# Performance work log

Measured on AMD Instinct MI355X. Metric: run time of the kernel, lower is better.

## Reference

```python
import jax, jax.numpy as jnp
import numpy as np


def _grouped_attn(q, k, v, mask, scale):
    # q: [T,H,D], k/v: [S,KH,D], mask: [T,S] or [KH,T,S] (True = visible)
    T, H, D = q.shape
    S, KH, _ = k.shape
    G = H // KH
    qg = q.reshape(T, KH, G, D)
    logits = jnp.einsum('tkgd,skd->kgts', qg, k) * scale
    if mask.ndim == 2:
        mask = jnp.broadcast_to(mask[None], (KH, T, S))
    logits = jnp.where(mask[:, None], logits, -1e30)
    p = jax.nn.softmax(logits, axis=-1)
    valid = mask.any(-1)  # [KH,T]: queries with at least one visible key
    p = jnp.where(valid[:, None, :, None], p, 0.0)
    o = jnp.einsum('kgts,skd->tkgd', p, v).reshape(T, H, D)
    return o, p


def setup_inputs() -> dict:
    key = jax.random.key(0)
    ks = jax.random.split(key, 4)
    T, H, KH, D = 2048, 16, 2, 128
    q = jax.random.normal(ks[0], (T, H, D), jnp.float32)
    k = jax.random.normal(ks[1], (T, KH, D), jnp.float32)
    v = jax.random.normal(ks[2], (T, KH, D), jnp.float32)
    w = jax.random.uniform(ks[3], (T, H, 3), jnp.float32)
    return dict(q=q, k=k, v=v, w=w, kernel_size=32, stride=16, block_size=64,
                top_n=16, num_init_blocks=1, num_local_blocks=2, window_size=512)


def reference(q, k, v, w, kernel_size, stride, block_size, top_n,
              num_init_blocks, num_local_blocks, window_size):
    T, H, D = q.shape
    KH = k.shape[1]
    scale = 1.0 / np.sqrt(D).astype(np.float32)
    t = jnp.arange(T)
    causal = t[None, :] <= t[:, None]  # [T,S]

    # ---- 1) compression: mean-pool overlapping windows of kernel_size / stride ----
    n_cmp = (T - kernel_size) // stride + 1
    starts = np.arange(n_cmp) * stride
    win_idx = starts[:, None] + np.arange(kernel_size)[None, :]  # [Ncmp,ks]
    cmp_k = k[win_idx].mean(axis=1)  # [Ncmp,KH,D]
    cmp_v = v[win_idx].mean(axis=1)
    j_end = jnp.asarray(starts) + kernel_size - 1
    cmp_mask = j_end[None, :] <= t[:, None]  # block fully in the past
    o_cmp, p_cmp = _grouped_attn(q, cmp_k, cmp_v, cmp_mask, scale)  # p_cmp [KH,G,T,Ncmp]

    # ---- 2) block selection from compressed attention probabilities ----
    n_blk = (T + block_size - 1) // block_size
    js, je = starts, starts + kernel_size
    bs_, be_ = np.arange(n_blk) * block_size, (np.arange(n_blk) + 1) * block_size
    M = jnp.asarray(((js[:, None] < be_[None, :]) & (bs_[None, :] < je[:, None])),
                    dtype=q.dtype)  # [Ncmp,Nblk] overlap indicator
    blk_score = jnp.einsum('kgtj,jb->ktb', p_cmp, M)  # sum over group heads

    b = jnp.arange(n_blk)
    t_blk = t // block_size
    forced = (b[None, :] < num_init_blocks) | \
             ((b[None, :] <= t_blk[:, None]) & (b[None, :] >= t_blk[:, None] - num_local_blocks + 1))
    blk_valid = (b[None, :] * block_size) <= t[:, None]
    score = jnp.where(forced[None], 1e30, blk_score)
    score = jnp.where(blk_valid[None], score, -1e30)
    _, idx = jax.lax.top_k(score, top_n)  # [KH,T,top_n]
    sel_blk = jax.nn.one_hot(idx, n_blk, dtype=q.dtype).sum(-2) > 0  # [KH,T,Nblk]

    # ---- 3) selected-block attention ----
    tok_sel = sel_blk[:, :, t // block_size]  # [KH,T,T]
    slc_mask = tok_sel & causal[None]
    o_slc, _ = _grouped_attn(q, k, v, slc_mask, scale)

    # ---- 4) sliding-window attention ----
    win_mask = causal & ((t[:, None] - t[None, :]) < window_size)
    o_win, _ = _grouped_attn(q, k, v, win_mask, scale)

    # ---- 5) gated combination ----
    o = w[..., 0:1] * o_cmp + w[..., 1:2] * o_slc + w[..., 2:3] * o_win
    return o
```

## Files before the change

kernel.cpp:

```cpp
#include <hip/hip_runtime.h>
#include <hip/hip_bf16.h>
#include <math.h>

#define T_ 2048
#define H_ 16
#define KH_ 2
#define G_ 8
#define D_ 128
#define NCMP 127
#define JP 128
#define NBLK 32
#define TOPN 16
#define WIN_ 512
#define SCALE 0.08838834764831845f

typedef __attribute__((ext_vector_type(8))) short short8;
typedef __attribute__((ext_vector_type(16))) float f32x16;

__device__ __forceinline__ unsigned short f2bf(float x) {
    union { float f; unsigned u; } c; c.f = x;
    unsigned u = c.u + 0x7fffu + ((c.u >> 16) & 1u);
    return (unsigned short)(u >> 16);
}
__device__ __forceinline__ float bf2f(unsigned short b) {
    union { unsigned u; float f; } c; c.u = (unsigned)b << 16; return c.f;
}

#define GLD16(gsrc, lds) \
    __builtin_amdgcn_global_load_lds( \
        (const __attribute__((address_space(1))) unsigned int*)(gsrc), \
        (__attribute__((address_space(3))) unsigned int*)(lds), 16, 0, 0)

__global__ __launch_bounds__(256) void prep_kv(
        const float* __restrict__ k, const float* __restrict__ v,
        unsigned short* __restrict__ kimg, unsigned short* __restrict__ vtimg) {
    const int b  = blockIdx.x;
    const int kh = blockIdx.y;
    const int s0 = b << 6;
    const int tid = threadIdx.x;
    const size_t tb = ((size_t)kh * 32 + b) * 8192;
#pragma unroll
    for (int it = 0; it < 4; ++it) {
        int idx = it * 256 + tid;
        int r = idx >> 4, c = idx & 15;
        const float* src = k + (size_t)(s0 + r) * (KH_ * D_) + kh * D_ + c * 8;
        float4 x = *reinterpret_cast<const float4*>(src);
        float4 y = *reinterpret_cast<const float4*>(src + 4);
        union { unsigned short u[8]; uint4 q; } o;
        o.u[0] = f2bf(x.x); o.u[1] = f2bf(x.y); o.u[2] = f2bf(x.z); o.u[3] = f2bf(x.w);
        o.u[4] = f2bf(y.x); o.u[5] = f2bf(y.y); o.u[6] = f2bf(y.z); o.u[7] = f2bf(y.w);
        *reinterpret_cast<uint4*>(&kimg[tb + r * 128 + ((c ^ (r & 7)) << 3)]) = o.q;
    }
#pragma unroll
    for (int it = 0; it < 4; ++it) {
        int idx = it * 256 + tid;
        int d = idx & 127, kc8 = idx >> 7;
        union { unsigned short u[8]; uint4 q; } o;
#pragma unroll
        for (int e = 0; e < 8; ++e)
            o.u[e] = f2bf(v[(size_t)(s0 + kc8 * 8 + e) * (KH_ * D_) + kh * D_ + d]);
        *reinterpret_cast<uint4*>(&vtimg[tb + d * 64 + ((kc8 ^ (d & 7)) << 3)]) = o.q;
    }
}

__global__ __launch_bounds__(128) void build_cmp(
        const float* __restrict__ k, const float* __restrict__ v,
        unsigned short* __restrict__ khiI, unsigned short* __restrict__ kloI,
        unsigned short* __restrict__ vflat) {
    int j  = blockIdx.x;
    int kh = blockIdx.y;
    int d  = threadIdx.x;
    unsigned short hb = 0, lb = 0, vb = 0;
    if (j < NCMP) {
        int s0 = j * 16;
        float sk = 0.f, sv = 0.f;
        for (int i = 0; i < 32; ++i) {
            sk += k[(size_t)(s0 + i) * KH_ * D_ + kh * D_ + d];
            sv += v[(size_t)(s0 + i) * KH_ * D_ + kh * D_ + d];
        }
        float mk = sk * (1.f / 32.f), mv = sv * (1.f / 32.f);
        hb = f2bf(mk);
        lb = f2bf(mk - bf2f(hb));
        vb = f2bf(mv);
    }
    int c = d >> 3;
    size_t ib = (size_t)kh * 16384 + j * 128 + ((c ^ (j & 7)) << 3) + (d & 7);
    khiI[ib] = hb;
    kloI[ib] = lb;
    vflat[(size_t)kh * 16384 + j * 128 + d] = vb;
}

__global__ __launch_bounds__(256) void prep_cmp_img(
        const unsigned short* __restrict__ vflat, unsigned short* __restrict__ cvtI) {
    const int kh = blockIdx.x;
    const int tid = threadIdx.x;
#pragma unroll
    for (int it = 0; it < 8; ++it) {
        int idx = it * 256 + tid;
        int d = idx & 127, jc8 = idx >> 7;
        union { unsigned short u[8]; uint4 q; } o;
#pragma unroll
        for (int e = 0; e < 8; ++e)
            o.u[e] = vflat[(size_t)kh * 16384 + (jc8 * 8 + e) * 128 + d];
        *reinterpret_cast<uint4*>(
            &cvtI[(size_t)kh * 16384 + d * 128 + ((jc8 ^ (d & 7)) << 3)]) = o.q;
    }
}

__global__ __launch_bounds__(256, 1) void cmp_attn_mfma(
        const float* __restrict__ q, const float* __restrict__ w,
        const unsigned short* __restrict__ khiI, const unsigned short* __restrict__ kloI,
        const unsigned short* __restrict__ cvtI,
        float* __restrict__ out, unsigned int* __restrict__ sel) {
    const int qt  = blockIdx.x;
    const int kh  = blockIdx.y;
    const int t0  = qt * 16;
    const int tid = threadIdx.x;
    const int wv  = tid >> 6;
    const int lane = tid & 63;
    const int l31 = lane & 31;
    const int hi  = lane >> 5;
    const int hi4 = hi * 4;

    __shared__ unsigned short KHI[JP * D_];
    __shared__ unsigned short KLO[JP * D_];
    __shared__ unsigned short CVT[JP * D_];
    __shared__ float wsc_s[16 * 132];
    __shared__ float bsc_s[16 * 32];
    __shared__ unsigned int sel_s[16];
    __shared__ float wfac[4][32];

    if (tid < 16) sel_s[tid] = 0u;
    for (int i = tid; i < 16 * 132; i += 256) wsc_s[i] = 0.f;

    const size_t cb = (size_t)kh * 16384;
#pragma unroll
    for (int it = 0; it < 8; ++it) {
        int off = (wv * 8 + it) * 512;
        GLD16(khiI + cb + off + lane * 8, &KHI[off]);
        GLD16(kloI + cb + off + lane * 8, &KLO[off]);
        GLD16(cvtI + cb + off + lane * 8, &CVT[off]);
    }

    const int qloc = l31 & 15;
    const int t    = t0 + qloc;
    const int h    = kh * G_ + 2 * wv + (l31 >> 4);
    short8 qhi[8], qlo[8];
    {
        const float* qrow = q + (size_t)t * (H_ * D_) + h * D_;
#pragma unroll
        for (int dc = 0; dc < 8; ++dc) {
            int d0 = dc * 16 + hi * 8;
            float4 x = *reinterpret_cast<const float4*>(qrow + d0);
            float4 y = *reinterpret_cast<const float4*>(qrow + d0 + 4);
            float e_[8] = {x.x, x.y, x.z, x.w, y.x, y.y, y.z, y.w};
            short8 fh, fl;
#pragma unroll
            for (int e = 0; e < 8; ++e) {
                unsigned short hb = f2bf(e_[e]);
                fh[e] = (short)hb;
                fl[e] = (short)f2bf(e_[e] - bf2f(hb));
            }
            qhi[dc] = fh; qlo[dc] = fl;
        }
    }
    __syncthreads();

    f32x16 s_[4];
#pragma unroll
    for (int tl = 0; tl < 4; ++tl)
#pragma unroll
        for (int r = 0; r < 16; ++r) s_[tl][r] = 0.f;
    __builtin_amdgcn_s_setprio(1);
#pragma unroll
    for (int dc = 0; dc < 8; ++dc) {
        int c8 = dc * 2 + hi;
        int swz = (c8 ^ (l31 & 7)) << 3;
#pragma unroll
        for (int tl = 0; tl < 4; ++tl) {
            int off = (tl * 32 + l31) * 128 + swz;
            short8 ahi = *reinterpret_cast<const short8*>(&KHI[off]);
            short8 alo = *reinterpret_cast<const short8*>(&KLO[off]);
            s_[tl] = __builtin_amdgcn_mfma_f32_32x32x16_bf16(ahi, qhi[dc], s_[tl], 0, 0, 0);
            s_[tl] = __builtin_amdgcn_mfma_f32_32x32x16_bf16(alo, qhi[dc], s_[tl], 0, 0, 0);
            s_[tl] = __builtin_amdgcn_mfma_f32_32x32x16_bf16(ahi, qlo[dc], s_[tl], 0, 0, 0);
        }
    }
    __builtin_amdgcn_s_setprio(0);

    const int nv = (t >= 31) ? (((t - 31) >> 4) + 1) : 0;
    float m = -1e30f;
#pragma unroll
    for (int tl = 0; tl < 4; ++tl)
#pragma unroll
        for (int r = 0; r < 16; ++r) {
            int j = tl * 32 + (r & 3) + 8 * (r >> 2) + hi4;
            float lg = (j < nv) ? s_[tl][r] * SCALE : -1e30f;
            s_[tl][r] = lg;
            m = fmaxf(m, lg);
        }
    m = fmaxf(m, __shfl_xor(m, 32));
    float lsum = 0.f;
#pragma unroll
    for (int tl = 0; tl < 4; ++tl)
#pragma unroll
        for (int r = 0; r < 16; ++r) {
            float e = __expf(s_[tl][r] - m);
            s_[tl][r] = e;
            lsum += e;
        }
    lsum += __shfl_xor(lsum, 32);
    const float linv = (nv > 0) ? 1.f / lsum : 0.f;

#pragma unroll
    for (int tl = 0; tl < 4; ++tl)
#pragma unroll
        for (int r = 0; r < 16; ++r) {
            int j = tl * 32 + (r & 3) + 8 * (r >> 2) + hi4;
            atomicAdd(&wsc_s[qloc * 132 + j], s_[tl][r] * linv);
        }

    f32x16 acc[4];
#pragma unroll
    for (int dt = 0; dt < 4; ++dt)
#pragma unroll
        for (int r = 0; r < 16; ++r) acc[dt][r] = 0.f;
#pragma unroll
    for (int kc = 0; kc < 8; ++kc) {
        const int su = kc >> 1, rb = (kc & 1) * 8;
        unsigned pa0, pa1, pb0, pb1;
        asm("v_cvt_pk_bf16_f32 %0, %1, %2" : "=v"(pa0) : "v"(s_[su][rb+0]), "v"(s_[su][rb+1]));
        asm("v_cvt_pk_bf16_f32 %0, %1, %2" : "=v"(pa1) : "v"(s_[su][rb+2]), "v"(s_[su][rb+3]));
        asm("v_cvt_pk_bf16_f32 %0, %1, %2" : "=v"(pb0) : "v"(s_[su][rb+4]), "v"(s_[su][rb+5]));
        asm("v_cvt_pk_bf16_f32 %0, %1, %2" : "=v"(pb1) : "v"(s_[su][rb+6]), "v"(s_[su][rb+7]));
        unsigned sa0 = __shfl_xor(pa0, 32);
        unsigned sa1 = __shfl_xor(pa1, 32);
        unsigned sb0 = __shfl_xor(pb0, 32);
        unsigned sb1 = __shfl_xor(pb1, 32);
        union { unsigned u[4]; short8 s8; } pa;
        pa.u[0] = hi ? sb0 : pa0;
        pa.u[1] = hi ? sb1 : pa1;
        pa.u[2] = hi ? pb0 : sa0;
        pa.u[3] = hi ? pb1 : sa1;
        const int jc8 = kc * 2 + hi;
        __builtin_amdgcn_s_setprio(1);
#pragma unroll
        for (int dt = 0; dt < 4; ++dt) {
            int d = dt * 32 + l31;
            short8 bf = *reinterpret_cast<const short8*>(
                &CVT[d * 128 + ((jc8 ^ (d & 7)) << 3)]);
            acc[dt] = __builtin_amdgcn_mfma_f32_32x32x16_bf16(pa.s8, bf, acc[dt], 0, 0, 0);
        }
        __builtin_amdgcn_s_setprio(0);
    }

    wfac[wv][l31] = w[(size_t)t * (H_ * 3) + h * 3 + 0] * linv;
    __syncthreads();

    float wfr[16];
#pragma unroll
    for (int r = 0; r < 16; ++r)
        wfr[r] = wfac[wv][(r & 3) + 8 * (r >> 2) + hi4];
#pragma unroll
    for (int dt = 0; dt < 4; ++dt)
#pragma unroll
        for (int r = 0; r < 16; ++r) {
            int crow = (r & 3) + 8 * (r >> 2) + hi4;
            int tt = t0 + (crow & 15);
            int hh = kh * G_ + 2 * wv + (crow >> 4);
            out[(size_t)tt * (H_ * D_) + hh * D_ + dt * 32 + l31] = acc[dt][r] * wfr[r];
        }

#pragma unroll
    for (int half = 0; half < 2; ++half) {
        int b  = (tid & 15) + half * 16;
        int qq = tid >> 4;
        int tt = t0 + qq;
        float sc = 0.f;
        int j0 = 4 * b - 1; if (j0 < 0) j0 = 0;
        int j1 = 4 * b + 3; if (j1 > NCMP - 1) j1 = NCMP - 1;
        for (int j = j0; j <= j1; ++j) sc += wsc_s[qq * 132 + j];
        int tb = tt >> 6;
        bool forced = (b == 0) || (b <= tb && b >= tb - 1);
        if (forced) sc = 1e30f;
        if (b * 64 > tt) sc = -1e30f;
        bsc_s[qq * 32 + b] = sc;
    }
    __syncthreads();

#pragma unroll
    for (int half = 0; half < 2; ++half) {
        int b  = (tid & 15) + half * 16;
        int qq = tid >> 4;
        float sb = bsc_s[qq * 32 + b];
        int cnt = 0;
        for (int b2 = 0; b2 < NBLK; ++b2) {
            float s2 = bsc_s[qq * 32 + b2];
            cnt += (s2 > sb) || (s2 == sb && b2 < b);
        }
        if (cnt < TOPN) atomicOr(&sel_s[qq], 1u << b);
    }
    __syncthreads();
    if (tid < 16) sel[kh * T_ + t0 + tid] = sel_s[tid];
}

__global__ __launch_bounds__(256, 2) void slc_win_mfma(
        const float* __restrict__ q, const unsigned short* __restrict__ kimg,
        const unsigned short* __restrict__ vtimg, const float* __restrict__ w,
        const unsigned int* __restrict__ sel, float* __restrict__ out,
        float* __restrict__ winb, float* __restrict__ slcb, int use_scratch) {
    const int phase = blockIdx.z;
    const int qt    = phase ? (gridDim.x - 1 - blockIdx.x) : blockIdx.x;
    const int kh    = blockIdx.y;
    const int t0    = qt * 16;
    const int tid   = threadIdx.x;
    const int wv    = tid >> 6;
    const int lane  = tid & 63;
    const int l31   = lane & 31;
    const int hi    = lane >> 5;
    const int hi4   = hi * 4;

    __shared__ unsigned short Kl[2][64 * 128];
    __shared__ unsigned short Vt[2][128 * 64];
    __shared__ float wfac[4][32];

    const int qloc = l31 & 15;
    const int t    = t0 + qloc;
    const int h    = kh * G_ + 2 * wv + (l31 >> 4);

    short8 qf[8];
    {
        const float* qrow = q + (size_t)t * (H_ * D_) + h * D_;
#pragma unroll
        for (int dc = 0; dc < 8; ++dc) {
            int d0 = dc * 16 + hi * 8;
            float4 x = *reinterpret_cast<const float4*>(qrow + d0);
            float4 y = *reinterpret_cast<const float4*>(qrow + d0 + 4);
            short8 f;
            f[0] = (short)f2bf(x.x); f[1] = (short)f2bf(x.y);
            f[2] = (short)f2bf(x.z); f[3] = (short)f2bf(x.w);
            f[4] = (short)f2bf(y.x); f[5] = (short)f2bf(y.y);
            f[6] = (short)f2bf(y.z); f[7] = (short)f2bf(y.w);
            qf[dc] = f;
        }
    }

    const unsigned int smask = sel[kh * T_ + t];
    const int tbmax = t0 >> 6;
    unsigned int rem = 0;
    int bidx = 0;
    if (phase == 0) {
        int lo = t0 - (WIN_ - 1); if (lo < 0) lo = 0;
        bidx = lo >> 6;
    } else {
        unsigned int vm = (tbmax >= 31) ? 0xffffffffu : ((2u << tbmax) - 1u);
        rem = smask;
        rem |= __shfl_xor(rem, 1); rem |= __shfl_xor(rem, 2);
        rem |= __shfl_xor(rem, 4); rem |= __shfl_xor(rem, 8);
        rem &= vm;
    }

    f32x16 acc[4];
#pragma unroll
    for (int dt = 0; dt < 4; ++dt)
#pragma unroll
        for (int r = 0; r < 16; ++r) acc[dt][r] = 0.f;
    float m_run = -1e30f, l_run = 0.f;

    int b_cur;
    if (phase == 0) b_cur = bidx++;
    else { b_cur = rem ? (__ffs(rem) - 1) : -1; if (rem) rem &= rem - 1; }

    if (b_cur >= 0) {
        const size_t tb = ((size_t)kh * 32 + b_cur) * 8192;
#pragma unroll
        for (int it = 0; it < 4; ++it) {
            int off = (wv * 4 + it) * 512;
            GLD16(kimg + tb + off + lane * 8, &Kl[0][off]);
            GLD16(vtimg + tb + off + lane * 8, &Vt[0][off]);
        }
    }
    __syncthreads();

    int cur = 0;
    while (b_cur >= 0) {
        int b_next;
        if (phase == 0) b_next = (bidx <= tbmax) ? bidx++ : -1;
        else { b_next = rem ? (__ffs(rem) - 1) : -1; if (rem) rem &= rem - 1; }

        if (b_next >= 0) {
            const size_t tb = ((size_t)kh * 32 + b_next) * 8192;
#pragma unroll
            for (int it = 0; it < 4; ++it) {
                int off = (wv * 4 + it) * 512;
                GLD16(kimg + tb + off + lane * 8, &Kl[cur ^ 1][off]);
                GLD16(vtimg + tb + off + lane * 8, &Vt[cur ^ 1][off]);
            }
        }

        const unsigned short* Kc = Kl[cur];
        const unsigned short* Vc = Vt[cur];
        const int s0 = b_cur << 6;

        f32x16 s_[2];
#pragma unroll
        for (int r = 0; r < 16; ++r) { s_[0][r] = 0.f; s_[1][r] = 0.f; }
        __builtin_amdgcn_s_setprio(1);
#pragma unroll
        for (int dc = 0; dc < 8; ++dc) {
            int c8 = dc * 2 + hi;
            int swz = (c8 ^ (l31 & 7)) << 3;
            short8 a0 = *reinterpret_cast<const short8*>(&Kc[l31 * 128 + swz]);
            short8 a1 = *reinterpret_cast<const short8*>(&Kc[(32 + l31) * 128 + swz]);
            s_[0] = __builtin_amdgcn_mfma_f32_32x32x16_bf16(a0, qf[dc], s_[0], 0, 0, 0);
            s_[1] = __builtin_amdgcn_mfma_f32_32x32x16_bf16(a1, qf[dc], s_[1], 0, 0, 0);
        }
        __builtin_amdgcn_s_setprio(0);

        const int sb = (smask >> b_cur) & 1;
        float p_[2][16];
        float mc = -INFINITY;
#pragma unroll
        for (int sub = 0; sub < 2; ++sub)
#pragma unroll
            for (int r = 0; r < 16; ++r) {
                int crow = (r & 3) + 8 * (r >> 2) + hi4;
                int s = s0 + sub * 32 + crow;
                bool ok = (s <= t) && (phase ? (sb != 0) : (s + WIN_ > t));
                float lg = ok ? s_[sub][r] * SCALE : -INFINITY;
                p_[sub][r] = lg;
                mc = fmaxf(mc, lg);
            }
        mc = fmaxf(mc, __shfl_xor(mc, 1));
        mc = fmaxf(mc, __shfl_xor(mc, 2));
        mc = fmaxf(mc, __shfl_xor(mc, 4));
        mc = fmaxf(mc, __shfl_xor(mc, 8));
        mc = fmaxf(mc, __shfl_xor(mc, 16));
        mc = fmaxf(mc, __shfl_xor(mc, 32));
        float mnew = fmaxf(m_run, mc);
        float f = __expf(m_run - mnew);
        float lsum = 0.f;
#pragma unroll
        for (int sub = 0; sub < 2; ++sub)
#pragma unroll
            for (int r = 0; r < 16; ++r) {
                float e = __expf(p_[sub][r] - mnew);
                p_[sub][r] = e;
                lsum += e;
            }
        lsum += __shfl_xor(lsum, 32);
        l_run = l_run * f + lsum;
        m_run = mnew;
#pragma unroll
        for (int dt = 0; dt < 4; ++dt)
#pragma unroll
            for (int r = 0; r < 16; ++r) acc[dt][r] *= f;

#pragma unroll
        for (int kc = 0; kc < 4; ++kc) {
            const int su = kc >> 1, rb = (kc & 1) * 8;
            unsigned pa0, pb0, pa1, pb1;
            asm("v_cvt_pk_bf16_f32 %0, %1, %2" : "=v"(pa0) : "v"(p_[su][rb+0]), "v"(p_[su][rb+1]));
            asm("v_cvt_pk_bf16_f32 %0, %1, %2" : "=v"(pa1) : "v"(p_[su][rb+2]), "v"(p_[su][rb+3]));
            asm("v_cvt_pk_bf16_f32 %0, %1, %2" : "=v"(pb0) : "v"(p_[su][rb+4]), "v"(p_[su][rb+5]));
            asm("v_cvt_pk_bf16_f32 %0, %1, %2" : "=v"(pb1) : "v"(p_[su][rb+6]), "v"(p_[su][rb+7]));
            unsigned sa0 = __shfl_xor(pa0, 32);
            unsigned sa1 = __shfl_xor(pa1, 32);
            unsigned sb0 = __shfl_xor(pb0, 32);
            unsigned sb1 = __shfl_xor(pb1, 32);
            union { unsigned u[4]; short8 s8; } pa;
            pa.u[0] = hi ? sb0 : pa0;
            pa.u[1] = hi ? sb1 : pa1;
            pa.u[2] = hi ? pb0 : sa0;
            pa.u[3] = hi ? pb1 : sa1;
            const int kc8 = kc * 2 + hi;
            __builtin_amdgcn_s_setprio(1);
#pragma unroll
            for (int dt = 0; dt < 4; ++dt) {
                int d = dt * 32 + l31;
                short8 bf = *reinterpret_cast<const short8*>(
                    &Vc[d * 64 + ((kc8 ^ (d & 7)) << 3)]);
                acc[dt] = __builtin_amdgcn_mfma_f32_32x32x16_bf16(pa.s8, bf, acc[dt], 0, 0, 0);
            }
            __builtin_amdgcn_s_setprio(0);
        }

        __syncthreads();
        b_cur = b_next;
        cur ^= 1;
    }

    float linv = 1.f / l_run;
    int widx = (phase == 0) ? 2 : 1;
    wfac[wv][l31] = w[(size_t)t * (H_ * 3) + h * 3 + widx] * linv;
    __syncthreads();
    float wfr[16];
#pragma unroll
    for (int r = 0; r < 16; ++r)
        wfr[r] = wfac[wv][(r & 3) + 8 * (r >> 2) + hi4];
    float* base = (phase == 0) ? winb : slcb;
#pragma unroll
    for (int dt = 0; dt < 4; ++dt)
#pragma unroll
        for (int r = 0; r < 16; ++r) {
            int crow = (r & 3) + 8 * (r >> 2) + hi4;
            int tt = t0 + (crow & 15);
            int hh = kh * G_ + 2 * wv + (crow >> 4);
            size_t idx = (size_t)tt * (H_ * D_) + hh * D_ + dt * 32 + l31;
            float val = acc[dt][r] * wfr[r];
            if (use_scratch) base[idx] = val;
            else             atomicAdd(&out[idx], val);
        }
}

__global__ __launch_bounds__(256) void combine_out(float* __restrict__ out,
        const float* __restrict__ a, const float* __restrict__ b) {
    int i = blockIdx.x * 256 + threadIdx.x;
    float4 o = reinterpret_cast<float4*>(out)[i];
    float4 x = reinterpret_cast<const float4*>(a)[i];
    float4 y = reinterpret_cast<const float4*>(b)[i];
    o.x += x.x + y.x; o.y += x.y + y.y; o.z += x.z + y.z; o.w += x.w + y.w;
    reinterpret_cast<float4*>(out)[i] = o;
}

extern "C" void kernel_launch(void* const* d_in, const int* in_sizes, int n_in,
                              void* d_out, int out_size, void* d_ws, size_t ws_size,
                              hipStream_t stream) {
    const float* q = (const float*)d_in[0];
    const float* k = (const float*)d_in[1];
    const float* v = (const float*)d_in[2];
    const float* w = (const float*)d_in[3];
    float* out = (float*)d_out;

    char* ws = (char*)d_ws;
    unsigned short* kimg  = (unsigned short*)(ws);
    unsigned short* vtimg = (unsigned short*)(ws + (1u << 20));
    unsigned short* khiI  = (unsigned short*)(ws + (2u << 20));
    unsigned short* kloI  = (unsigned short*)(ws + (2u << 20) + 65536);
    unsigned short* cvtI  = (unsigned short*)(ws + (2u << 20) + 2 * 65536);
    unsigned short* vflat = (unsigned short*)(ws + (2u << 20) + 3 * 65536);
    unsigned int*   sel   = (unsigned int*)(ws + (2u << 20) + 4 * 65536);
    float* winb_s = (float*)(ws + (2u << 20) + 4 * 65536 + 16384);
    float* slcb_s = winb_s + (size_t)T_ * H_ * D_;
    const size_t need = (2u << 20) + 4 * 65536 + 16384
                        + 2 * (size_t)T_ * H_ * D_ * sizeof(float);
    const int use_scratch = (ws_size >= need) ? 1 : 0;
    float* winb = use_scratch ? winb_s : out;
    float* slcb = use_scratch ? slcb_s : out;

    hipLaunchKernelGGL(prep_kv, dim3(32, KH_), dim3(256), 0, stream, k, v, kimg, vtimg);
    hipLaunchKernelGGL(build_cmp, dim3(128, KH_), dim3(128), 0, stream,
                       k, v, khiI, kloI, vflat);
    hipLaunchKernelGGL(prep_cmp_img, dim3(KH_), dim3(256), 0, stream, vflat, cvtI);
    hipLaunchKernelGGL(cmp_attn_mfma, dim3(T_ / 16, KH_), dim3(256), 0, stream,
                       q, w, khiI, kloI, cvtI, out, sel);
    hipLaunchKernelGGL(slc_win_mfma, dim3(T_ / 16, KH_, 2), dim3(256), 0, stream,
                       q, kimg, vtimg, w, sel, out, winb, slcb, use_scratch);
    if (use_scratch) {
        hipLaunchKernelGGL(combine_out, dim3((T_ * H_ * D_ / 4) / 256), dim3(256), 0, stream,
                           out, winb, slcb);
    }
}
```

Before: 258.7 us.

## Split head groups across blocks, drop double buffering, add lazy-rescale exp2 softmax

The selected/window attention kernel now uses 128-thread blocks, each covering four heads instead of eight, and launches twice as many blocks. The double-buffered K/V LDS staging becomes a single buffer loaded synchronously at the start of each iteration. The softmax folds scale·log2e into Q and uses raw v_exp_f32. It skips masking on interior blocks and rescales only when the running max grows past a threshold. This trades less LDS per block and cheaper softmax for losing load/compute overlap, and each block now reloads K/V that was previously shared by all eight heads.

```diff
diff --git a/kernel.cpp b/kernel.cpp
--- a/kernel.cpp
+++ b/kernel.cpp
@@ -13,6 +13,8 @@
 #define TOPN 16
 #define WIN_ 512
 #define SCALE 0.08838834764831845f
+#define SCL2 (0.08838834764831845f * 1.4426950408889634f)
+#define THR2 11.541560f
 
 typedef __attribute__((ext_vector_type(8))) short short8;
 typedef __attribute__((ext_vector_type(16))) float f32x16;
@@ -24,6 +26,11 @@
 }
 __device__ __forceinline__ float bf2f(unsigned short b) {
     union { unsigned u; float f; } c; c.u = (unsigned)b << 16; return c.f;
+}
+__device__ __forceinline__ float exp2_fast(float x) {
+    float r;
+    asm("v_exp_f32 %0, %1" : "=v"(r) : "v"(x));
+    return r;
 }
 
 #define GLD16(gsrc, lds) \
@@ -304,13 +311,14 @@
     if (tid < 16) sel[kh * T_ + t0 + tid] = sel_s[tid];
 }
 
-__global__ __launch_bounds__(256, 2) void slc_win_mfma(
+__global__ __launch_bounds__(128, 2) void slc_win_mfma(
         const float* __restrict__ q, const unsigned short* __restrict__ kimg,
         const unsigned short* __restrict__ vtimg, const float* __restrict__ w,
         const unsigned int* __restrict__ sel, float* __restrict__ out,
         float* __restrict__ winb, float* __restrict__ slcb, int use_scratch) {
-    const int phase = blockIdx.z;
-    const int qt    = phase ? (gridDim.x - 1 - blockIdx.x) : blockIdx.x;
+    const int phase = blockIdx.z >> 1;
+    const int hpair = blockIdx.z & 1;
+    const int qt    = phase ? ((int)gridDim.x - 1 - (int)blockIdx.x) : (int)blockIdx.x;
     const int kh    = blockIdx.y;
     const int t0    = qt * 16;
     const int tid   = threadIdx.x;
@@ -320,13 +328,14 @@
     const int hi    = lane >> 5;
     const int hi4   = hi * 4;
 
-    __shared__ unsigned short Kl[2][64 * 128];
-    __shared__ unsigned short Vt[2][128 * 64];
-    __shared__ float wfac[4][32];
+    __shared__ unsigned short Kl[64 * 128];
+    __shared__ unsigned short Vt[128 * 64];
+    __shared__ float wfac[2][32];
 
     const int qloc = l31 & 15;
     const int t    = t0 + qloc;
-    const int h    = kh * G_ + 2 * wv + (l31 >> 4);
+    const int hloc = hpair * 4 + wv * 2 + (l31 >> 4);
+    const int h    = kh * G_ + hloc;
 
     short8 qf[8];
     {
@@ -337,10 +346,10 @@
             float4 x = *reinterpret_cast<const float4*>(qrow + d0);
             float4 y = *reinterpret_cast<const float4*>(qrow + d0 + 4);
             short8 f;
-            f[0] = (short)f2bf(x.x); f[1] = (short)f2bf(x.y);
-            f[2] = (short)f2bf(x.z); f[3] = (short)f2bf(x.w);
-            f[4] = (short)f2bf(y.x); f[5] = (short)f2bf(y.y);
-            f[6] = (short)f2bf(y.z); f[7] = (short)f2bf(y.w);
+            f[0] = (short)f2bf(x.x * SCL2); f[1] = (short)f2bf(x.y * SCL2);
+            f[2] = (short)f2bf(x.z * SCL2); f[3] = (short)f2bf(x.w * SCL2);
+            f[4] = (short)f2bf(y.x * SCL2); f[5] = (short)f2bf(y.y * SCL2);
+            f[6] = (short)f2bf(y.z * SCL2); f[7] = (short)f2bf(y.w * SCL2);
             qf[dc] = f;
         }
     }
@@ -371,35 +380,23 @@
     if (phase == 0) b_cur = bidx++;
     else { b_cur = rem ? (__ffs(rem) - 1) : -1; if (rem) rem &= rem - 1; }
 
-    if (b_cur >= 0) {
-        const size_t tb = ((size_t)kh * 32 + b_cur) * 8192;
-#pragma unroll
-        for (int it = 0; it < 4; ++it) {
-            int off = (wv * 4 + it) * 512;
-            GLD16(kimg + tb + off + lane * 8, &Kl[0][off]);
-            GLD16(vtimg + tb + off + lane * 8, &Vt[0][off]);
-        }
-    }
-    __syncthreads();
-
-    int cur = 0;
     while (b_cur >= 0) {
-        int b_next;
-        if (phase == 0) b_next = (bidx <= tbmax) ? bidx++ : -1;
-        else { b_next = rem ? (__ffs(rem) - 1) : -1; if (rem) rem &= rem - 1; }
-
-        if (b_next >= 0) {
-            const size_t tb = ((size_t)kh * 32 + b_next) * 8192;
-#pragma unroll
-            for (int it = 0; it < 4; ++it) {
-                int off = (wv * 4 + it) * 512;
-                GLD16(kimg + tb + off + lane * 8, &Kl[cur ^ 1][off]);
-                GLD16(vtimg + tb + off + lane * 8, &Vt[cur ^ 1][off]);
+        __syncthreads();
+        {
+            const size_t tb = ((size_t)kh * 32 + b_cur) * 8192;
+#pragma unroll
+            for (int it = 0; it < 8; ++it) {
+                int off = (wv * 8 + it) * 512;
+                GLD16(kimg + tb + off + lane * 8, &Kl[off]);
             }
-        }
-
-        const unsigned short* Kc = Kl[cur];
-        const unsigned short* Vc = Vt[cur];
+#pragma unroll
+            for (int it = 0; it < 8; ++it) {
+                int off = (wv * 8 + it) * 512;
+                GLD16(vtimg + tb + off + lane * 8, &Vt[off]);
+            }
+        }
+        __syncthreads();
+
         const int s0 = b_cur << 6;
 
         f32x16 s_[2];
@@ -410,84 +407,105 @@
         for (int dc = 0; dc < 8; ++dc) {
             int c8 = dc * 2 + hi;
             int swz = (c8 ^ (l31 & 7)) << 3;
-            short8 a0 = *reinterpret_cast<const short8*>(&Kc[l31 * 128 + swz]);
-            short8 a1 = *reinterpret_cast<const short8*>(&Kc[(32 + l31) * 128 + swz]);
+            short8 a0 = *reinterpret_cast<const short8*>(&Kl[l31 * 128 + swz]);
+            short8 a1 = *reinterpret_cast<const short8*>(&Kl[(32 + l31) * 128 + swz]);
             s_[0] = __builtin_amdgcn_mfma_f32_32x32x16_bf16(a0, qf[dc], s_[0], 0, 0, 0);
             s_[1] = __builtin_amdgcn_mfma_f32_32x32x16_bf16(a1, qf[dc], s_[1], 0, 0, 0);
         }
         __builtin_amdgcn_s_setprio(0);
 
         const int sb = (smask >> b_cur) & 1;
-        float p_[2][16];
-        float mc = -INFINITY;
+        const bool needmask = (b_cur == tbmax) ||
+                              ((phase == 0) && (s0 + 496 < t0));
+        float mc = -1e30f;
+        if (needmask) {
+#pragma unroll
+            for (int sub = 0; sub < 2; ++sub)
+#pragma unroll
+                for (int r = 0; r < 16; ++r) {
+                    int crow = (r & 3) + 8 * (r >> 2) + hi4;
+                    int s = s0 + sub * 32 + crow;
+                    bool ok = (s <= t) && (phase ? (sb != 0) : (s + WIN_ > t));
+                    float lg = ok ? s_[sub][r] : -1e30f;
+                    s_[sub][r] = lg;
+                    mc = fmaxf(mc, lg);
+                }
+        } else {
+#pragma unroll
+            for (int sub = 0; sub < 2; ++sub)
+#pragma unroll
+                for (int r = 0; r < 16; ++r) mc = fmaxf(mc, s_[sub][r]);
+            if (phase) mc = sb ? mc : -1e30f;
+        }
+
+        float f = 1.f;
+        const bool resc = !__all(mc <= m_run + THR2);
+        if (resc) {
+            float wm = mc;
+            wm = fmaxf(wm, __shfl_xor(wm, 1));
+            wm = fmaxf(wm, __shfl_xor(wm, 2));
+            wm = fmaxf(wm, __shfl_xor(wm, 4));
+            wm = fmaxf(wm, __shfl_xor(wm, 8));
+            wm = fmaxf(wm, __shfl_xor(wm, 16));
+            wm = fmaxf(wm, __shfl_xor(wm, 32));
+            float mnew = fmaxf(m_run, wm);
+            f = exp2_fast(m_run - mnew);
+            m_run = mnew;
+        }
+
+        float lsum = 0.f;
 #pragma unroll
         for (int sub = 0; sub < 2; ++sub)
 #pragma unroll
             for (int r = 0; r < 16; ++r) {
-                int crow = (r & 3) + 8 * (r >> 2) + hi4;
-                int s = s0 + sub * 32 + crow;
-                bool ok = (s <= t) && (phase ? (sb != 0) : (s + WIN_ > t));
-                float lg = ok ? s_[sub][r] * SCALE : -INFINITY;
-                p_[sub][r] = lg;
-                mc = fmaxf(mc, lg);
-            }
-        mc = fmaxf(mc, __shfl_xor(mc, 1));
-        mc = fmaxf(mc, __shfl_xor(mc, 2));
-        mc = fmaxf(mc, __shfl_xor(mc, 4));
-        mc = fmaxf(mc, __shfl_xor(mc, 8));
-        mc = fmaxf(mc, __shfl_xor(mc, 16));
-        mc = fmaxf(mc, __shfl_xor(mc, 32));
-        float mnew = fmaxf(m_run, mc);
-        float f = __expf(m_run - mnew);
-        float lsum = 0.f;
-#pragma unroll
-        for (int sub = 0; sub < 2; ++sub)
-#pragma unroll
-            for (int r = 0; r < 16; ++r) {
-                float e = __expf(p_[sub][r] - mnew);
-                p_[sub][r] = e;
+                float e = exp2_fast(s_[sub][r] - m_run);
+                s_[sub][r] = e;
                 lsum += e;
             }
+        if (phase && !sb) lsum = 0.f;
         lsum += __shfl_xor(lsum, 32);
-        l_run = l_run * f + lsum;
-        m_run = mnew;
-#pragma unroll
-        for (int dt = 0; dt < 4; ++dt)
-#pragma unroll
-            for (int r = 0; r < 16; ++r) acc[dt][r] *= f;
-
+        if (resc) {
+            l_run = l_run * f + lsum;
+#pragma unroll
+            for (int dt = 0; dt < 4; ++dt)
+#pragma unroll
+                for (int r = 0; r < 16; ++r) acc[dt][r] *= f;
+        } else {
+            l_run += lsum;
+        }
+
+        const unsigned zm = (phase && !sb) ? 0u : 0xffffffffu;
 #pragma unroll
         for (int kc = 0; kc < 4; ++kc) {
             const int su = kc >> 1, rb = (kc & 1) * 8;
             unsigned pa0, pb0, pa1, pb1;
-            asm("v_cvt_pk_bf16_f32 %0, %1, %2" : "=v"(pa0) : "v"(p_[su][rb+0]), "v"(p_[su][rb+1]));
-            asm("v_cvt_pk_bf16_f32 %0, %1, %2" : "=v"(pa1) : "v"(p_[su][rb+2]), "v"(p_[su][rb+3]));
-            asm("v_cvt_pk_bf16_f32 %0, %1, %2" : "=v"(pb0) : "v"(p_[su][rb+4]), "v"(p_[su][rb+5]));
-            asm("v_cvt_pk_bf16_f32 %0, %1, %2" : "=v"(pb1) : "v"(p_[su][rb+6]), "v"(p_[su][rb+7]));
+            asm("v_cvt_pk_bf16_f32 %0, %1, %2" : "=v"(pa0) : "v"(s_[su][rb+0]), "v"(s_[su][rb+1]));
+            asm("v_cvt_pk_bf16_f32 %0, %1, %2" : "=v"(pa1) : "v"(s_[su][rb+2]), "v"(s_[su][rb+3]));
+            asm("v_cvt_pk_bf16_f32 %0, %1, %2" : "=v"(pb0) : "v"(s_[su][rb+4]), "v"(s_[su][rb+5]));
+            asm("v_cvt_pk_bf16_f32 %0, %1, %2" : "=v"(pb1) : "v"(s_[su][rb+6]), "v"(s_[su][rb+7]));
             unsigned sa0 = __shfl_xor(pa0, 32);
             unsigned sa1 = __shfl_xor(pa1, 32);
             unsigned sb0 = __shfl_xor(pb0, 32);
             unsigned sb1 = __shfl_xor(pb1, 32);
             union { unsigned u[4]; short8 s8; } pa;
-            pa.u[0] = hi ? sb0 : pa0;
-            pa.u[1] = hi ? sb1 : pa1;
-            pa.u[2] = hi ? pb0 : sa0;
-            pa.u[3] = hi ? pb1 : sa1;
+            pa.u[0] = (hi ? sb0 : pa0) & zm;
+            pa.u[1] = (hi ? sb1 : pa1) & zm;
+            pa.u[2] = (hi ? pb0 : sa0) & zm;
+            pa.u[3] = (hi ? pb1 : sa1) & zm;
             const int kc8 = kc * 2 + hi;
             __builtin_amdgcn_s_setprio(1);
 #pragma unroll
             for (int dt = 0; dt < 4; ++dt) {
                 int d = dt * 32 + l31;
                 short8 bf = *reinterpret_cast<const short8*>(
-                    &Vc[d * 64 + ((kc8 ^ (d & 7)) << 3)]);
+                    &Vt[d * 64 + ((kc8 ^ (d & 7)) << 3)]);
                 acc[dt] = __builtin_amdgcn_mfma_f32_32x32x16_bf16(pa.s8, bf, acc[dt], 0, 0, 0);
             }
             __builtin_amdgcn_s_setprio(0);
         }
 
-        __syncthreads();
-        b_cur = b_next;
-        cur ^= 1;
+        if (phase == 0) b_cur = (bidx <= tbmax) ? bidx++ : -1;
+        else { b_cur = rem ? (__ffs(rem) - 1) : -1; if (rem) rem &= rem - 1; }
     }
 
     float linv = 1.f / l_run;
@@ -505,7 +523,7 @@
         for (int r = 0; r < 16; ++r) {
             int crow = (r & 3) + 8 * (r >> 2) + hi4;
             int tt = t0 + (crow & 15);
-            int hh = kh * G_ + 2 * wv + (crow >> 4);
+            int hh = kh * G_ + hpair * 4 + wv * 2 + (crow >> 4);
             size_t idx = (size_t)tt * (H_ * D_) + hh * D_ + dt * 32 + l31;
             float val = acc[dt][r] * wfr[r];
             if (use_scratch) base[idx] = val;
@@ -554,7 +572,7 @@
     hipLaunchKernelGGL(prep_cmp_img, dim3(KH_), dim3(256), 0, stream, vflat, cvtI);
     hipLaunchKernelGGL(cmp_attn_mfma, dim3(T_ / 16, KH_), dim3(256), 0, stream,
                        q, w, khiI, kloI, cvtI, out, sel);
-    hipLaunchKernelGGL(slc_win_mfma, dim3(T_ / 16, KH_, 2), dim3(256), 0, stream,
+    hipLaunchKernelGGL(slc_win_mfma, dim3(T_ / 16, KH_, 4), dim3(128), 0, stream,
                        q, kimg, vtimg, w, sel, out, winb, slcb, use_scratch);
     if (use_scratch) {
         hipLaunchKernelGGL(combine_out, dim3((T_ * H_ * D_ / 4) / 256), dim3(256), 0, stream,
```

Result: faster. 226.4 us (-12.5%).
